# Performance work log

Measured on AMD Instinct MI355X. Metric: run time of the kernel, lower is better.

The kernel has to match this reference:

```python
import jax, jax.numpy as jnp
import numpy as np
from jax import lax

P = 8  # patch size

def _to_patches(x):
    # [B,C,H,W] -> [B,C,H//P,W//P,P,P]
    b, c, h, w = x.shape
    x = x.reshape(b, c, h // P, P, w // P, P)
    return x.transpose(0, 1, 2, 4, 3, 5)

def _from_patches(x):
    # [B,C,h,w,P,P] -> [B,C,h*P,w*P]
    b, c, h, w, p1, p2 = x.shape
    return x.transpose(0, 1, 2, 4, 3, 5).reshape(b, c, h * p1, w * p2)

def setup_inputs() -> dict:
    key = jax.random.key(0)
    ks = jax.random.split(key, 7)
    B, C = 4, 64
    H = W = 256
    HID2 = 2 * C  # hidden_features * 2 with expansion factor 1
    img = jax.random.normal(ks[0], (B, C, H, W), dtype=jnp.float32)
    event = jax.random.normal(ks[1], (B, C, H, W), dtype=jnp.float32)
    # conv weights (no bias), OIHW
    w_img = jax.random.normal(ks[2], (HID2, C, 1, 1), dtype=jnp.float32) * (1.0 / np.sqrt(C))
    w_event = jax.random.normal(ks[3], (HID2, C, 1, 1), dtype=jnp.float32) * (1.0 / np.sqrt(C))
    w_dw = jax.random.normal(ks[4], (HID2, 1, 3, 3), dtype=jnp.float32) * (1.0 / 3.0)
    fft_filter = jnp.ones((HID2, 1, 1, P, P // 2 + 1), dtype=jnp.float32)  # init = ones, as in module
    w_out = jax.random.normal(ks[5], (C, C, 1, 1), dtype=jnp.float32) * (1.0 / np.sqrt(C))
    return {"img": img, "event": event, "w_img": w_img, "w_event": w_event,
            "w_dw": w_dw, "fft_filter": fft_filter, "w_out": w_out}

def reference(img, event, w_img, w_event, w_dw, fft_filter, w_out):
    hid2 = w_img.shape[0]
    # 1x1 input convs (no bias) as einsum
    img_ = jnp.einsum('bchw,oc->bohw', img, w_img[:, :, 0, 0])
    event_ = jnp.einsum('bchw,oc->bohw', event, w_event[:, :, 0, 0])
    # 8x8 patchwise rfft2
    img_fft = jnp.fft.rfft2(_to_patches(img_))        # [B,2C,h,w,8,5] complex
    event_fft = jnp.fft.rfft2(_to_patches(event_))
    event_fft = event_fft * fft_filter                 # filter broadcasts over h,w
    x_fft = img_fft * event_fft + event_fft
    x_patch = jnp.fft.irfft2(x_fft, s=(P, P))
    x = _from_patches(x_patch)                          # [B,2C,H,W]
    # depthwise 3x3 conv, groups = 2C
    x = lax.conv_general_dilated(x, w_dw, window_strides=(1, 1), padding='SAME',
                                 feature_group_count=hid2,
                                 dimension_numbers=('NCHW', 'OIHW', 'NCHW'))
    x1, x2 = jnp.split(x, 2, axis=1)
    x = jax.nn.gelu(x1, approximate=False) * x2
    # 1x1 project out
    return jnp.einsum('bchw,oc->bohw', x, w_out[:, :, 0, 0])
```

## Files before the change

kernel.cpp:

```cpp
#include <hip/hip_runtime.h>
#include <math.h>

typedef unsigned short u16;
typedef unsigned int   u32;

#define S2 0.70710678118654752440f

typedef float f32x4 __attribute__((ext_vector_type(4)));
typedef short bf16x8 __attribute__((ext_vector_type(8)));
typedef float f32x2 __attribute__((ext_vector_type(2)));
typedef __bf16 bf16x2 __attribute__((ext_vector_type(2)));
#define MFMA(a,b,c) __builtin_amdgcn_mfma_f32_16x16x32_bf16(a,b,c,0,0,0)

__device__ __forceinline__ float bf2f(u16 u){
  union { u32 i; float f; } v; v.i = ((u32)u) << 16; return v.f;
}
__device__ __forceinline__ u16 f2bf(float f){
  union { __bf16 b; u16 u; } v; v.b = (__bf16)f; return v.u;
}
__device__ __forceinline__ u32 pk_bf16(float lo, float hi){
  f32x2 s; s.x = lo; s.y = hi;
  union { bf16x2 h; u32 u; } v;
  v.h = __builtin_convertvector(s, bf16x2);
  return v.u;
}

struct C2 { float r, i; };

__device__ __forceinline__ void fft8_fwd(C2* y){
  C2 a0 = {y[0].r+y[4].r, y[0].i+y[4].i};
  C2 a1 = {y[0].r-y[4].r, y[0].i-y[4].i};
  C2 a2 = {y[2].r+y[6].r, y[2].i+y[6].i};
  C2 a3 = {y[2].r-y[6].r, y[2].i-y[6].i};
  C2 b0 = {y[1].r+y[5].r, y[1].i+y[5].i};
  C2 b1 = {y[1].r-y[5].r, y[1].i-y[5].i};
  C2 b2 = {y[3].r+y[7].r, y[3].i+y[7].i};
  C2 b3 = {y[3].r-y[7].r, y[3].i-y[7].i};
  C2 E0 = {a0.r+a2.r, a0.i+a2.i};
  C2 E2 = {a0.r-a2.r, a0.i-a2.i};
  C2 E1 = {a1.r+a3.i, a1.i-a3.r};
  C2 E3 = {a1.r-a3.i, a1.i+a3.r};
  C2 O0 = {b0.r+b2.r, b0.i+b2.i};
  C2 O2 = {b0.r-b2.r, b0.i-b2.i};
  C2 O1 = {b1.r+b3.i, b1.i-b3.r};
  C2 O3 = {b1.r-b3.i, b1.i+b3.r};
  C2 t1 = {S2*(O1.r+O1.i), S2*(O1.i-O1.r)};
  C2 t2 = {O2.i, -O2.r};
  C2 t3 = {S2*(O3.i-O3.r), -S2*(O3.r+O3.i)};
  y[0].r=E0.r+O0.r; y[0].i=E0.i+O0.i;
  y[4].r=E0.r-O0.r; y[4].i=E0.i-O0.i;
  y[1].r=E1.r+t1.r; y[1].i=E1.i+t1.i;
  y[5].r=E1.r-t1.r; y[5].i=E1.i-t1.i;
  y[2].r=E2.r+t2.r; y[2].i=E2.i+t2.i;
  y[6].r=E2.r-t2.r; y[6].i=E2.i-t2.i;
  y[3].r=E3.r+t3.r; y[3].i=E3.i+t3.i;
  y[7].r=E3.r-t3.r; y[7].i=E3.i-t3.i;
}

__device__ __forceinline__ void fft8_inv(C2* z){
  C2 A0 = {z[0].r+z[4].r, z[0].i+z[4].i};
  C2 A1 = {z[1].r+z[5].r, z[1].i+z[5].i};
  C2 A2 = {z[2].r+z[6].r, z[2].i+z[6].i};
  C2 A3 = {z[3].r+z[7].r, z[3].i+z[7].i};
  C2 D0 = {z[0].r-z[4].r, z[0].i-z[4].i};
  C2 D1 = {z[1].r-z[5].r, z[1].i-z[5].i};
  C2 D2 = {z[2].r-z[6].r, z[2].i-z[6].i};
  C2 D3 = {z[3].r-z[7].r, z[3].i-z[7].i};
  C2 B0 = D0;
  C2 B1 = {S2*(D1.r-D1.i), S2*(D1.i+D1.r)};
  C2 B2 = {-D2.i, D2.r};
  C2 B3 = {-S2*(D3.r+D3.i), S2*(D3.r-D3.i)};
  z[0].r = A0.r+A1.r+A2.r+A3.r;           z[0].i = A0.i+A1.i+A2.i+A3.i;
  z[2].r = A0.r-A2.r-(A1.i-A3.i);         z[2].i = A0.i-A2.i+(A1.r-A3.r);
  z[4].r = A0.r-A1.r+A2.r-A3.r;           z[4].i = A0.i-A1.i+A2.i-A3.i;
  z[6].r = A0.r-A2.r+(A1.i-A3.i);         z[6].i = A0.i-A2.i-(A1.r-A3.r);
  z[1].r = B0.r+B1.r+B2.r+B3.r;           z[1].i = B0.i+B1.i+B2.i+B3.i;
  z[3].r = B0.r-B2.r-(B1.i-B3.i);         z[3].i = B0.i-B2.i+(B1.r-B3.r);
  z[5].r = B0.r-B1.r+B2.r-B3.r;           z[5].i = B0.i-B1.i+B2.i-B3.i;
  z[7].r = B0.r-B2.r+(B1.i-B3.i);         z[7].i = B0.i-B2.i-(B1.r-B3.r);
}

__device__ __forceinline__ void rfft8_row(float* x){
  float et0=x[0]+x[4], et1=x[0]-x[4], et2=x[2]+x[6], et3=x[2]-x[6];
  float ot0=x[1]+x[5], ot1=x[1]-x[5], ot2=x[3]+x[7], ot3=x[3]-x[7];
  float E0=et0+et2, E2=et0-et2;
  float O0=ot0+ot2, O2=ot0-ot2;
  float om=S2*(ot1-ot3), op=S2*(ot1+ot3);
  x[0]=E0+O0;  x[1]=E0-O0;
  x[2]=et1+om; x[3]=-et3-op;
  x[4]=E2;     x[5]=-O2;
  x[6]=et1-om; x[7]=et3-op;
}

__device__ __forceinline__ void irfft8_row(float f0, C2 R1, C2 R2, C2 R3, float f4, float* x){
  float A0  = f0+f4, B0v = f0-f4;
  float A1r = R1.r+R3.r, A1i = R1.i-R3.i;
  float A2  = 2.f*R2.r;
  float D1r = R1.r-R3.r, D1i = R1.i+R3.i;
  float B1r = S2*(D1r-D1i), B1i = S2*(D1i+D1r);
  float B2  = -2.f*R2.i;
  const float k = 1.f/64.f;
  x[0]=k*(A0 +A2+2.f*A1r); x[2]=k*(A0 -A2-2.f*A1i);
  x[4]=k*(A0 +A2-2.f*A1r); x[6]=k*(A0 -A2+2.f*A1i);
  x[1]=k*(B0v+B2+2.f*B1r); x[3]=k*(B0v-B2-2.f*B1i);
  x[5]=k*(B0v+B2-2.f*B1r); x[7]=k*(B0v-B2+2.f*B1i);
}

__global__ void k_prep(const float* __restrict__ wi, const float* __restrict__ we,
                       const float* __restrict__ wo,
                       u16* __restrict__ wbi, u16* __restrict__ wbe, u16* __restrict__ wbo){
  int i = blockIdx.x*256 + threadIdx.x;
  if (i < 8192)        wbi[i]        = f2bf(wi[i]);
  else if (i < 16384)  wbe[i-8192]   = f2bf(we[i-8192]);
  else if (i < 20480)  wbo[i-16384]  = f2bf(wo[i-16384]);
}

__global__ __launch_bounds__(256, 2)
void k_front(const float* __restrict__ img, const float* __restrict__ evt,
             const u16* __restrict__ wbi, const u16* __restrict__ wbe,
             const float* __restrict__ filt, u16* __restrict__ yout){
  __shared__ __align__(16) u16 s_a[8192];
  __shared__ __align__(16) u16 s_spec[16384];

  const int t   = threadIdx.x;
  const int bid = blockIdx.x;
  const int b   = bid >> 9;
  const int ph  = (bid >> 4) & 31;
  const int bx  = bid & 15;
  const int wv   = t >> 6;
  const int quad = (t >> 4) & 3;
  const int ln15 = t & 15;
  const int pc   = t >> 7;
  const int c    = t & 127;

  auto stage_load = [&](const float* src, float4* v){
    #pragma unroll
    for (int i=0;i<8;i++){
      int task = t + 256*i;
      int ci = task>>5, q = task&31;
      int r = q>>2, j = q&3;
      v[i] = *(const float4*)(src +
          (((size_t)(b*64+ci)*256 + ph*8 + r)*256 + bx*16 + j*4));
    }
  };
  auto stage_write = [&](const float4* v){
    #pragma unroll
    for (int i=0;i<8;i++){
      int task = t + 256*i;
      int ci = task>>5, q = task&31;
      int r = q>>2, j = q&3;
      int p0 = (j>>1)*64 + r*8 + (j&1)*4;
      int gbase = ci>>3, cl = ci&7;
      float vv[4] = {v[i].x, v[i].y, v[i].z, v[i].w};
      #pragma unroll
      for (int w=0;w<4;w++){
        int p = p0+w;
        int g = gbase ^ (p&7) ^ r;
        s_a[p*64 + g*8 + cl] = f2bf(vv[w]);
      }
    }
  };

  auto do_gemm = [&](const u16* __restrict__ wb){
    f32x4 acc[2][8];
    #pragma unroll
    for (int nt=0;nt<2;nt++)
      #pragma unroll
      for (int mt=0;mt<8;mt++)
        acc[nt][mt] = (f32x4){0.f,0.f,0.f,0.f};
    const int nb = wv*32;
    #pragma unroll
    for (int kk=0;kk<2;kk++){
      bf16x8 bf0 = *(const bf16x8*)&wb[(nb      + ln15)*64 + kk*32 + quad*8];
      bf16x8 bf1 = *(const bf16x8*)&wb[(nb + 16 + ln15)*64 + kk*32 + quad*8];
      #pragma unroll
      for (int mt=0;mt<8;mt++){
        int pix = mt*16 + ln15;
        int g = (kk*4+quad) ^ (pix&7) ^ ((pix>>3)&7);
        bf16x8 af = *(const bf16x8*)&s_a[pix*64 + g*8];
        acc[0][mt] = MFMA(af, bf0, acc[0][mt]);
        acc[1][mt] = MFMA(af, bf1, acc[1][mt]);
      }
    }
    #pragma unroll
    for (int nt=0;nt<2;nt++){
      int och = nb + nt*16 + ln15;
      #pragma unroll
      for (int mt=0;mt<8;mt++){
        int p0 = mt*16 + quad*4;
        f32x4 v = acc[nt][mt];
        u32 lo = pk_bf16(v.x, v.y);
        u32 hi = pk_bf16(v.z, v.w);
        int d = (p0>>3) ^ (och&7);
        u32* dst = (u32*)&s_spec[och*128 + d*8 + (p0&7)];
        dst[0] = lo; dst[1] = hi;
      }
    }
  };

  auto read_spec = [&](float* p){
    #pragma unroll
    for (int d=0; d<8; d++){
      int cz = (pc*8+d) ^ (c&7);
      const uint4 q4 = *(const uint4*)&s_spec[c*128 + cz*8];
      u32 ws4[4] = {q4.x, q4.y, q4.z, q4.w};
      #pragma unroll
      for (int e=0;e<4;e++){
        p[d*8+2*e]   = bf2f((u16)(ws4[e] & 0xFFFFu));
        p[d*8+2*e+1] = bf2f((u16)(ws4[e] >> 16));
      }
    }
  };

  {
    float4 sv[8];
    stage_load(evt, sv);
    stage_write(sv);
  }
  __syncthreads();
  do_gemm(wbe);
  __syncthreads();

  float4 sv[8];
  stage_load(img, sv);

  float pe[64];
  read_spec(pe);
  #pragma unroll
  for (int r=0;r<8;r++) rfft8_row(&pe[r*8]);

  stage_write(sv);
  __syncthreads();
  do_gemm(wbi);
  __syncthreads();

  float pi[64];
  read_spec(pi);
  __syncthreads();
  #pragma unroll
  for (int r=0;r<8;r++) rfft8_row(&pi[r*8]);

  C2 X[8][5];
  {
    const float* fl = filt + c*40;
    #pragma unroll
    for (int j=0;j<5;j++){
      C2 e8[8], i8[8];
      #pragma unroll
      for (int r=0;r<8;r++){
        float re_e, im_e, re_i, im_i;
        if (j==0){ re_e=pe[r*8];   im_e=0.f; re_i=pi[r*8];   im_i=0.f; }
        else if (j==4){ re_e=pe[r*8+1]; im_e=0.f; re_i=pi[r*8+1]; im_i=0.f; }
        else { re_e=pe[r*8+2*j]; im_e=pe[r*8+2*j+1];
               re_i=pi[r*8+2*j]; im_i=pi[r*8+2*j+1]; }
        e8[r].r=re_e; e8[r].i=im_e; i8[r].r=re_i; i8[r].i=im_i;
      }
      fft8_fwd(e8);
      fft8_fwd(i8);
      #pragma unroll
      for (int ky=0;ky<8;ky++){
        float f  = fl[ky*5+j];
        float fr = e8[ky].r*f, fi2 = e8[ky].i*f;
        X[ky][j].r = i8[ky].r*fr - i8[ky].i*fi2 + fr;
        X[ky][j].i = i8[ky].r*fi2 + i8[ky].i*fr + fi2;
      }
    }
    #pragma unroll
    for (int j=0;j<5;j++){
      C2 z[8];
      #pragma unroll
      for (int ky=0;ky<8;ky++) z[ky] = X[ky][j];
      fft8_inv(z);
      #pragma unroll
      for (int ky=0;ky<8;ky++) X[ky][j] = z[ky];
    }
  }

  {
    const int cp = (c&31) | ((c&32)<<1) | ((c&64)>>1);
    #pragma unroll
    for (int r=0;r<8;r++){
      float xr[8];
      irfft8_row(X[r][0].r, X[r][1], X[r][2], X[r][3], X[r][4].r, xr);
      #pragma unroll
      for (int n2=0;n2<8;n2++)
        s_spec[(pc*64 + r*8 + n2)*128 + cp] = f2bf(xr[n2]);
    }
  }
  __syncthreads();

  {
    const uint4* sg = (const uint4*)s_spec;
    uint4* dst = (uint4*)(yout + (size_t)(b*1024 + ph*32 + bx*2)*8192);
    #pragma unroll
    for (int i=0;i<8;i++){
      int q2 = t + 256*i;
      dst[q2] = sg[q2];
    }
  }
}

__global__ __launch_bounds__(256, 2)
void k_back(const u16* __restrict__ y, const float* __restrict__ wdw,
            const u16* __restrict__ wbo, float* __restrict__ out){
  __shared__ __align__(16) u16 L[18*19*68];
  __shared__ __align__(16) u16 A[256*32];

  const int t   = threadIdx.x;
  const int bid = blockIdx.x;
  const int b   = bid >> 8;
  const int ty  = (bid >> 4) & 15;
  const int tx  = bid & 15;
  const int wv   = t >> 6;
  const int quad = (t >> 4) & 3;
  const int ln15 = t & 15;
  const int y_  = t >> 4, x_ = t & 15;
  const int sw  = (t&3) ^ ((t>>2)&3);

  auto halo_load = [&](int chunk, uint4* hv){
    #pragma unroll
    for (int i=0;i<11;i++){
      int task = t + 256*i;
      uint4 v = make_uint4(0u,0u,0u,0u);
      if (task < 2592){
        int q = task & 7, pix = task >> 3;
        int py = pix/18, px = pix - py*18;
        int gy = ty*16 - 1 + py, gx = tx*16 - 1 + px;
        if ((unsigned)gy < 256u && (unsigned)gx < 256u){
          int phh = gy>>3, pww = gx>>3, k = (gy&7)*8 + (gx&7);
          v = *(const uint4*)&y[(((size_t)(b*1024 + phh*32 + pww))*64 + k)*128
                                + chunk*64 + q*8];
        }
      }
      hv[i] = v;
    }
  };
  auto halo_write = [&](const uint4* hv){
    #pragma unroll
    for (int i=0;i<11;i++){
      int task = t + 256*i;
      if (task < 2592){
        int q = task & 7, pix = task >> 3;
        int py = pix/18, px = pix - py*18;
        int ad = (py*19+px)*68 + q*8;
        *(uint2*)&L[ad]     = make_uint2(hv[i].x, hv[i].y);
        *(uint2*)&L[ad + 4] = make_uint2(hv[i].z, hv[i].w);
      }
    }
  };

  auto dwconv = [&](int chunk){
    #pragma unroll
    for (int cg=0; cg<8; cg++){
      float d1[4] = {0.f,0.f,0.f,0.f};
      float d2[4] = {0.f,0.f,0.f,0.f};
      const float* w1p = wdw + (chunk*32 + cg*4)*9;
      const float* w2p = wdw + (64 + chunk*32 + cg*4)*9;
      #pragma unroll
      for (int dy=0; dy<3; dy++)
        #pragma unroll
        for (int dx=0; dx<3; dx++){
          int base = ((y_+dy)*19 + (x_+dx))*68;
          const uint2 a1 = *(const uint2*)&L[base + cg*4];
          const uint2 a2 = *(const uint2*)&L[base + 32 + cg*4];
          const float* wp1 = w1p + dy*3 + dx;
          const float* wp2 = w2p + dy*3 + dx;
          d1[0] = fmaf(wp1[0],  bf2f((u16)(a1.x & 0xFFFFu)), d1[0]);
          d1[1] = fmaf(wp1[9],  bf2f((u16)(a1.x >> 16)),     d1[1]);
          d1[2] = fmaf(wp1[18], bf2f((u16)(a1.y & 0xFFFFu)), d1[2]);
          d1[3] = fmaf(wp1[27], bf2f((u16)(a1.y >> 16)),     d1[3]);
          d2[0] = fmaf(wp2[0],  bf2f((u16)(a2.x & 0xFFFFu)), d2[0]);
          d2[1] = fmaf(wp2[9],  bf2f((u16)(a2.x >> 16)),     d2[1]);
          d2[2] = fmaf(wp2[18], bf2f((u16)(a2.y & 0xFFFFu)), d2[2]);
          d2[3] = fmaf(wp2[27], bf2f((u16)(a2.y >> 16)),     d2[3]);
        }
      float gg[4];
      #pragma unroll
      for (int l=0;l<4;l++){
        float g1 = d1[l];
        float u  = 0.7978845608028654f * fmaf(0.044715f*g1*g1, g1, g1);
        float e  = __expf(2.f*u);
        float th = 1.f - 2.f*__builtin_amdgcn_rcpf(e + 1.f);
        float g  = 0.5f * g1 * (1.f + th);
        gg[l] = g * d2[l];
      }
      int pos = ((cg>>1) ^ sw)*8 + (cg&1)*4;
      *(uint2*)&A[t*32 + pos] =
          make_uint2(pk_bf16(gg[0], gg[1]), pk_bf16(gg[2], gg[3]));
    }
  };

  auto do_gemm = [&](int chunk, f32x4 (&acc)[4][4]){
    bf16x8 bfr[4];
    #pragma unroll
    for (int nt=0;nt<4;nt++)
      bfr[nt] = *(const bf16x8*)&wbo[(nt*16 + ln15)*64 + chunk*32 + quad*8];
    #pragma unroll
    for (int mt=0;mt<4;mt++){
      int px8 = wv*64 + mt*16 + ln15;
      int q2 = quad ^ ((px8&3) ^ ((px8>>2)&3));
      bf16x8 af = *(const bf16x8*)&A[px8*32 + q2*8];
      #pragma unroll
      for (int nt=0;nt<4;nt++)
        acc[mt][nt] = MFMA(af, bfr[nt], acc[mt][nt]);
    }
  };

  f32x4 acc[4][4];
  #pragma unroll
  for (int mt=0;mt<4;mt++)
    #pragma unroll
    for (int nt=0;nt<4;nt++)
      acc[mt][nt] = (f32x4){0.f,0.f,0.f,0.f};

  uint4 hv[11];
  halo_load(0, hv);
  halo_write(hv);
  __syncthreads();

  halo_load(1, hv);
  dwconv(0);
  __syncthreads();
  do_gemm(0, acc);
  halo_write(hv);
  __syncthreads();

  dwconv(1);
  __syncthreads();
  do_gemm(1, acc);

  #pragma unroll
  for (int mt=0;mt<4;mt++){
    int row = ty*16 + wv*4 + mt;
    #pragma unroll
    for (int nt=0;nt<4;nt++){
      int och = nt*16 + ln15;
      f32x4 v = acc[mt][nt];
      float4 o4 = make_float4(v.x, v.y, v.z, v.w);
      *(float4*)(out + (((size_t)(b*64 + och))*256 + row)*256 + tx*16 + quad*4) = o4;
    }
  }
}

extern "C" void kernel_launch(void* const* d_in, const int* in_sizes, int n_in,
                              void* d_out, int out_size, void* d_ws, size_t ws_size,
                              hipStream_t stream){
  const float* img   = (const float*)d_in[0];
  const float* evt   = (const float*)d_in[1];
  const float* w_img = (const float*)d_in[2];
  const float* w_evt = (const float*)d_in[3];
  const float* w_dw  = (const float*)d_in[4];
  const float* filt  = (const float*)d_in[5];
  const float* w_out = (const float*)d_in[6];
  float* out = (float*)d_out;

  u16* wbi = (u16*)d_ws;
  u16* wbe = (u16*)((char*)d_ws + 16384);
  u16* wbo = (u16*)((char*)d_ws + 32768);
  u16* y   = (u16*)((char*)d_ws + 65536);

  k_prep<<<80, 256, 0, stream>>>(w_img, w_evt, w_out, wbi, wbe, wbo);
  k_front<<<2048, 256, 0, stream>>>(img, evt, wbi, wbe, filt, y);
  k_back<<<1024, 256, 0, stream>>>(y, w_dw, wbo, out);
}
```

Baseline: 292.9 us.

## Drop weight prep kernel, convert fp32 weights inline, store front output directly

Measured after the change: 299.6 us. +2.3%, slower.

```diff
diff --git a/kernel.cpp b/kernel.cpp
--- a/kernel.cpp
+++ b/kernel.cpp
@@ -106,18 +106,9 @@
   x[5]=k*(B0v+B2-2.f*B1r); x[7]=k*(B0v-B2+2.f*B1i);
 }
 
-__global__ void k_prep(const float* __restrict__ wi, const float* __restrict__ we,
-                       const float* __restrict__ wo,
-                       u16* __restrict__ wbi, u16* __restrict__ wbe, u16* __restrict__ wbo){
-  int i = blockIdx.x*256 + threadIdx.x;
-  if (i < 8192)        wbi[i]        = f2bf(wi[i]);
-  else if (i < 16384)  wbe[i-8192]   = f2bf(we[i-8192]);
-  else if (i < 20480)  wbo[i-16384]  = f2bf(wo[i-16384]);
-}
-
 __global__ __launch_bounds__(256, 2)
 void k_front(const float* __restrict__ img, const float* __restrict__ evt,
-             const u16* __restrict__ wbi, const u16* __restrict__ wbe,
+             const float* __restrict__ wif, const float* __restrict__ wef,
              const float* __restrict__ filt, u16* __restrict__ yout){
   __shared__ __align__(16) u16 s_a[8192];
   __shared__ __align__(16) u16 s_spec[16384];
@@ -161,7 +152,17 @@
     }
   };
 
-  auto do_gemm = [&](const u16* __restrict__ wb){
+  auto ldw = [&](const float* wf, int row, int kk) -> bf16x8 {
+    const float* p = wf + row*64 + kk*32 + quad*8;
+    float4 a = *(const float4*)p;
+    float4 d = *(const float4*)(p+4);
+    union { u32 u[4]; bf16x8 v; } r;
+    r.u[0] = pk_bf16(a.x, a.y); r.u[1] = pk_bf16(a.z, a.w);
+    r.u[2] = pk_bf16(d.x, d.y); r.u[3] = pk_bf16(d.z, d.w);
+    return r.v;
+  };
+
+  auto do_gemm = [&](const float* __restrict__ wf){
     f32x4 acc[2][8];
     #pragma unroll
     for (int nt=0;nt<2;nt++)
@@ -171,8 +172,8 @@
     const int nb = wv*32;
     #pragma unroll
     for (int kk=0;kk<2;kk++){
-      bf16x8 bf0 = *(const bf16x8*)&wb[(nb      + ln15)*64 + kk*32 + quad*8];
-      bf16x8 bf1 = *(const bf16x8*)&wb[(nb + 16 + ln15)*64 + kk*32 + quad*8];
+      bf16x8 bf0 = ldw(wf, nb      + ln15, kk);
+      bf16x8 bf1 = ldw(wf, nb + 16 + ln15, kk);
       #pragma unroll
       for (int mt=0;mt<8;mt++){
         int pix = mt*16 + ln15;
@@ -218,7 +219,7 @@
     stage_write(sv);
   }
   __syncthreads();
-  do_gemm(wbe);
+  do_gemm(wef);
   __syncthreads();
 
   float4 sv[8];
@@ -231,12 +232,11 @@
 
   stage_write(sv);
   __syncthreads();
-  do_gemm(wbi);
+  do_gemm(wif);
   __syncthreads();
 
   float pi[64];
   read_spec(pi);
-  __syncthreads();
   #pragma unroll
   for (int r=0;r<8;r++) rfft8_row(&pi[r*8]);
 
@@ -278,31 +278,21 @@
 
   {
     const int cp = (c&31) | ((c&32)<<1) | ((c&64)>>1);
+    u16* ybase = yout + (size_t)(b*1024 + ph*32 + bx*2 + pc)*8192 + cp;
     #pragma unroll
     for (int r=0;r<8;r++){
       float xr[8];
       irfft8_row(X[r][0].r, X[r][1], X[r][2], X[r][3], X[r][4].r, xr);
       #pragma unroll
       for (int n2=0;n2<8;n2++)
-        s_spec[(pc*64 + r*8 + n2)*128 + cp] = f2bf(xr[n2]);
-    }
-  }
-  __syncthreads();
-
-  {
-    const uint4* sg = (const uint4*)s_spec;
-    uint4* dst = (uint4*)(yout + (size_t)(b*1024 + ph*32 + bx*2)*8192);
-    #pragma unroll
-    for (int i=0;i<8;i++){
-      int q2 = t + 256*i;
-      dst[q2] = sg[q2];
+        ybase[(r*8 + n2)*128] = f2bf(xr[n2]);
     }
   }
 }
 
 __global__ __launch_bounds__(256, 2)
 void k_back(const u16* __restrict__ y, const float* __restrict__ wdw,
-            const u16* __restrict__ wbo, float* __restrict__ out){
+            const float* __restrict__ wof, float* __restrict__ out){
   __shared__ __align__(16) u16 L[18*19*68];
   __shared__ __align__(16) u16 A[256*32];
 
@@ -393,8 +383,15 @@
   auto do_gemm = [&](int chunk, f32x4 (&acc)[4][4]){
     bf16x8 bfr[4];
     #pragma unroll
-    for (int nt=0;nt<4;nt++)
-      bfr[nt] = *(const bf16x8*)&wbo[(nt*16 + ln15)*64 + chunk*32 + quad*8];
+    for (int nt=0;nt<4;nt++){
+      const float* p = wof + (nt*16 + ln15)*64 + chunk*32 + quad*8;
+      float4 a = *(const float4*)p;
+      float4 d = *(const float4*)(p+4);
+      union { u32 u[4]; bf16x8 v; } r;
+      r.u[0] = pk_bf16(a.x, a.y); r.u[1] = pk_bf16(a.z, a.w);
+      r.u[2] = pk_bf16(d.x, d.y); r.u[3] = pk_bf16(d.z, d.w);
+      bfr[nt] = r.v;
+    }
     #pragma unroll
     for (int mt=0;mt<4;mt++){
       int px8 = wv*64 + mt*16 + ln15;
@@ -454,12 +451,8 @@
   const float* w_out = (const float*)d_in[6];
   float* out = (float*)d_out;
 
-  u16* wbi = (u16*)d_ws;
-  u16* wbe = (u16*)((char*)d_ws + 16384);
-  u16* wbo = (u16*)((char*)d_ws + 32768);
-  u16* y   = (u16*)((char*)d_ws + 65536);
-
-  k_prep<<<80, 256, 0, stream>>>(w_img, w_evt, w_out, wbi, wbe, wbo);
-  k_front<<<2048, 256, 0, stream>>>(img, evt, wbi, wbe, filt, y);
-  k_back<<<1024, 256, 0, stream>>>(y, w_dw, wbo, out);
-}
+  u16* y = (u16*)d_ws;
+
+  k_front<<<2048, 256, 0, stream>>>(img, evt, w_img, w_evt, filt, y);
+  k_back<<<1024, 256, 0, stream>>>(y, w_dw, w_out, out);
+}
```

## Restructure dwconv LDS layout to channel-planar, use 128-bit loads and packed FMA

Applied to the files above, without the earlier changes.

After: 294.8 us. About the same (+0.6%).

```diff
diff --git a/kernel.cpp b/kernel.cpp
--- a/kernel.cpp
+++ b/kernel.cpp
@@ -236,7 +236,6 @@
 
   float pi[64];
   read_spec(pi);
-  __syncthreads();
   #pragma unroll
   for (int r=0;r<8;r++) rfft8_row(&pi[r*8]);
 
@@ -276,6 +275,8 @@
     }
   }
 
+  __syncthreads();
+
   {
     const int cp = (c&31) | ((c&32)<<1) | ((c&64)>>1);
     #pragma unroll
@@ -303,7 +304,7 @@
 __global__ __launch_bounds__(256, 2)
 void k_back(const u16* __restrict__ y, const float* __restrict__ wdw,
             const u16* __restrict__ wbo, float* __restrict__ out){
-  __shared__ __align__(16) u16 L[18*19*68];
+  __shared__ __align__(16) u16 L[8*18*19*8];
   __shared__ __align__(16) u16 A[256*32];
 
   const int t   = threadIdx.x;
@@ -342,51 +343,56 @@
       if (task < 2592){
         int q = task & 7, pix = task >> 3;
         int py = pix/18, px = pix - py*18;
-        int ad = (py*19+px)*68 + q*8;
-        *(uint2*)&L[ad]     = make_uint2(hv[i].x, hv[i].y);
-        *(uint2*)&L[ad + 4] = make_uint2(hv[i].z, hv[i].w);
+        *(uint4*)&L[((q*18 + py)*19 + px)*8] = hv[i];
       }
     }
   };
 
   auto dwconv = [&](int chunk){
     #pragma unroll
-    for (int cg=0; cg<8; cg++){
-      float d1[4] = {0.f,0.f,0.f,0.f};
-      float d2[4] = {0.f,0.f,0.f,0.f};
-      const float* w1p = wdw + (chunk*32 + cg*4)*9;
-      const float* w2p = wdw + (64 + chunk*32 + cg*4)*9;
+    for (int cp=0; cp<4; cp++){
+      f32x2 d1v[4], d2v[4];
+      #pragma unroll
+      for (int k=0;k<4;k++){ d1v[k]=(f32x2){0.f,0.f}; d2v[k]=(f32x2){0.f,0.f}; }
+      const float* w1p = wdw + (chunk*32 + cp*8)*9;
+      const float* w2p = wdw + (64 + chunk*32 + cp*8)*9;
       #pragma unroll
       for (int dy=0; dy<3; dy++)
         #pragma unroll
         for (int dx=0; dx<3; dx++){
-          int base = ((y_+dy)*19 + (x_+dx))*68;
-          const uint2 a1 = *(const uint2*)&L[base + cg*4];
-          const uint2 a2 = *(const uint2*)&L[base + 32 + cg*4];
-          const float* wp1 = w1p + dy*3 + dx;
-          const float* wp2 = w2p + dy*3 + dx;
-          d1[0] = fmaf(wp1[0],  bf2f((u16)(a1.x & 0xFFFFu)), d1[0]);
-          d1[1] = fmaf(wp1[9],  bf2f((u16)(a1.x >> 16)),     d1[1]);
-          d1[2] = fmaf(wp1[18], bf2f((u16)(a1.y & 0xFFFFu)), d1[2]);
-          d1[3] = fmaf(wp1[27], bf2f((u16)(a1.y >> 16)),     d1[3]);
-          d2[0] = fmaf(wp2[0],  bf2f((u16)(a2.x & 0xFFFFu)), d2[0]);
-          d2[1] = fmaf(wp2[9],  bf2f((u16)(a2.x >> 16)),     d2[1]);
-          d2[2] = fmaf(wp2[18], bf2f((u16)(a2.y & 0xFFFFu)), d2[2]);
-          d2[3] = fmaf(wp2[27], bf2f((u16)(a2.y >> 16)),     d2[3]);
+          const int tap = dy*3 + dx;
+          const uint4 a1 = *(const uint4*)&L[(( cp   *18 + y_+dy)*19 + (x_+dx))*8];
+          const uint4 a2 = *(const uint4*)&L[(((cp+4)*18 + y_+dy)*19 + (x_+dx))*8];
+          const u32 u1[4] = {a1.x,a1.y,a1.z,a1.w};
+          const u32 u2[4] = {a2.x,a2.y,a2.z,a2.w};
+          #pragma unroll
+          for (int k=0;k<4;k++){
+            f32x2 x1, x2, wa, wb;
+            x1.x = bf2f((u16)(u1[k] & 0xFFFFu)); x1.y = bf2f((u16)(u1[k] >> 16));
+            x2.x = bf2f((u16)(u2[k] & 0xFFFFu)); x2.y = bf2f((u16)(u2[k] >> 16));
+            wa.x = w1p[(2*k)*9 + tap];  wa.y = w1p[(2*k+1)*9 + tap];
+            wb.x = w2p[(2*k)*9 + tap];  wb.y = w2p[(2*k+1)*9 + tap];
+            d1v[k] = d1v[k] + wa*x1;
+            d2v[k] = d2v[k] + wb*x2;
+          }
         }
-      float gg[4];
-      #pragma unroll
-      for (int l=0;l<4;l++){
-        float g1 = d1[l];
-        float u  = 0.7978845608028654f * fmaf(0.044715f*g1*g1, g1, g1);
-        float e  = __expf(2.f*u);
-        float th = 1.f - 2.f*__builtin_amdgcn_rcpf(e + 1.f);
-        float g  = 0.5f * g1 * (1.f + th);
-        gg[l] = g * d2[l];
-      }
-      int pos = ((cg>>1) ^ sw)*8 + (cg&1)*4;
-      *(uint2*)&A[t*32 + pos] =
-          make_uint2(pk_bf16(gg[0], gg[1]), pk_bf16(gg[2], gg[3]));
+      float gg[8];
+      #pragma unroll
+      for (int k=0;k<4;k++){
+        #pragma unroll
+        for (int h=0; h<2; h++){
+          float g1 = h ? d1v[k].y : d1v[k].x;
+          float dd = h ? d2v[k].y : d2v[k].x;
+          float uu = 0.7978845608028654f * fmaf(0.044715f*g1*g1, g1, g1);
+          float e  = __expf(2.f*uu);
+          float th = 1.f - 2.f*__builtin_amdgcn_rcpf(e + 1.f);
+          gg[2*k+h] = 0.5f * g1 * (1.f + th) * dd;
+        }
+      }
+      int pos = (cp ^ sw)*8;
+      *(uint4*)&A[t*32 + pos] =
+          make_uint4(pk_bf16(gg[0],gg[1]), pk_bf16(gg[2],gg[3]),
+                     pk_bf16(gg[4],gg[5]), pk_bf16(gg[6],gg[7]));
     }
   };
 
```
